# Kernel tuning notes

Measured on AMD Instinct MI355X. Metric: run time of the kernel, lower is better.

## Reference

```python
import jax, jax.numpy as jnp
import numpy as np

# ADMM hyperparameters for mode='only_tv'
GAMMA_TV = 10.0
ALPHA = 5.0
LAMBDA_TV = 1e-4
N_ITERS = 50


def soft_thresh(v, t):
    return jnp.sign(v) * jnp.maximum(jnp.abs(v) - t, 0.0)


def setup_inputs() -> dict:
    key = jax.random.key(0)
    k1, k2, k3 = jax.random.split(key, 3)
    target = jax.random.normal(k1, (4096,), dtype=jnp.float32)
    A = jax.random.normal(k2, (9, 4096), dtype=jnp.float32)  # [M, N], post-transpose
    x0 = jax.random.normal(k3, (4096,), dtype=jnp.float32)   # replaces torch.randn_like
    return {"target": target, "A": A, "x0": x0}


def reference(target, A, x0):
    N = A.shape[1]
    I = jnp.eye(N, dtype=A.dtype)
    Delta = jnp.roll(I, 1, axis=1) - I               # [N, N] circular difference
    DtD = Delta.T @ Delta
    AtA = A.T @ A
    # only_tv: gamma_l1 = beta = 0, so regularizer is ATA + gamma_tv*DtD + alpha*I
    inv_item = jnp.linalg.inv(AtA + GAMMA_TV * DtD + ALPHA * I)

    b = A @ target            # [M]
    bA = b @ A                # [N], constant across iterations

    def step(carry, _):
        x, eta_tv, tau = carry
        # u_tv: soft-threshold of backward difference (roll along axis 0)
        u_tv = soft_thresh(jnp.roll(x, 1, axis=0) - x + eta_tv / GAMMA_TV,
                           LAMBDA_TV / GAMMA_TV)
        # w: nonnegativity split variable
        w = jnp.maximum(x + tau / ALPHA, 0.0)
        # x-update (zero terms for l1/dwt/z dropped: gamma_l1 = gamma_dwt = beta = 0)
        resid = bA + (GAMMA_TV * u_tv - eta_tv) + (ALPHA * w - tau)
        x = resid @ inv_item
        # dual updates
        eta_tv = eta_tv + GAMMA_TV * (Delta @ x - u_tv)
        tau = tau + ALPHA * (x - w)
        return (x, eta_tv, tau), None

    zeros = jnp.zeros_like(x0)
    (x, _, _), _ = jax.lax.scan(step, (x0, zeros, zeros), None, length=N_ITERS)
    return x
```

## Files before the change

### kernel.cpp

```cpp
#include <hip/hip_runtime.h>
#include <math.h>

#define NT 512
#define EPT 8
#define NN 4096
#define MM 9
#define NIT 50
#define CJ 5

__device__ __forceinline__ void block_reduce9(const float pq[MM], float* __restrict__ s_part,
                                              float* __restrict__ dest, int destStride,
                                              int identCol, int t) {
#pragma unroll
  for (int m = 0; m < MM; ++m) s_part[m * NT + t] = pq[m];
  __syncthreads();
  const int wave = t >> 6, lane = t & 63;
  for (int m = wave; m < MM; m += NT / 64) {
    float s = 0.f;
#pragma unroll
    for (int k = 0; k < NT / 64; ++k) s += s_part[m * NT + lane + 64 * k];
#pragma unroll
    for (int off = 32; off; off >>= 1) s += __shfl_xor(s, off, 64);
    if (lane == 0) dest[m * destStride] = s + ((m == identCol) ? 1.f : 0.f);
  }
  __syncthreads();
}

__device__ __forceinline__ void solveM(const float r[EPT], float p[EPT],
                                       float* __restrict__ s_lastA,
                                       float* __restrict__ s_lastB, int t) {
  float yl[EPT];
  yl[EPT - 1] = r[EPT - 1] * 0.1f;
#pragma unroll
  for (int j = EPT - 2; j >= 0; --j) yl[j] = fmaf(0.5f, yl[j + 1], r[j] * 0.1f);
  s_lastA[t] = yl[0];
  __syncthreads();
  float c = 0.f, wgt = 1.f;
#pragma unroll
  for (int j = 0; j < CJ; ++j) { c = fmaf(wgt, s_lastA[(t + 1 + j) & (NT - 1)], c); wgt *= (1.f / 256.f); }
  float y[EPT];
  float f = 0.5f;
#pragma unroll
  for (int j = EPT - 1; j >= 0; --j) { y[j] = fmaf(c, f, yl[j]); f *= 0.5f; }
  float pl[EPT];
  pl[0] = 0.5f * y[0];
#pragma unroll
  for (int j = 1; j < EPT; ++j) pl[j] = 0.5f * (y[j] + pl[j - 1]);
  s_lastB[t] = pl[EPT - 1];
  __syncthreads();
  float c2 = 0.f, w2 = 1.f;
#pragma unroll
  for (int j = 0; j < CJ; ++j) { c2 = fmaf(w2, s_lastB[(t + NT - 1 - j) & (NT - 1)], c2); w2 *= (1.f / 256.f); }
  float f2 = 0.5f;
#pragma unroll
  for (int j = 0; j < EPT; ++j) { p[j] = fmaf(c2, f2, pl[j]); f2 *= 0.5f; }
}

__global__ void __launch_bounds__(NT)
admm_kernel(const float* __restrict__ tg, const float* __restrict__ Ag,
            const float* __restrict__ x0, float* __restrict__ out) {
  __shared__ float s_x[NN];
  __shared__ float s_part[MM * NT];
  __shared__ float s_lastA[NT];
  __shared__ float s_lastB[NT];
  __shared__ float s_q[MM];
  __shared__ float s_z[MM];
  __shared__ float s_S[MM * MM];
  __shared__ float s_Sinv[MM * MM];

  const int t = threadIdx.x;
  const int base = t * EPT;

  float A[MM][EPT];
#pragma unroll
  for (int m = 0; m < MM; ++m) {
    float4 a0 = *(const float4*)(Ag + m * NN + base);
    float4 a1 = *(const float4*)(Ag + m * NN + base + 4);
    A[m][0] = a0.x; A[m][1] = a0.y; A[m][2] = a0.z; A[m][3] = a0.w;
    A[m][4] = a1.x; A[m][5] = a1.y; A[m][6] = a1.z; A[m][7] = a1.w;
  }

  float x[EPT], tgt[EPT];
  {
    float4 v0 = *(const float4*)(x0 + base);
    float4 v1 = *(const float4*)(x0 + base + 4);
    x[0] = v0.x; x[1] = v0.y; x[2] = v0.z; x[3] = v0.w;
    x[4] = v1.x; x[5] = v1.y; x[6] = v1.z; x[7] = v1.w;
    float4 t0 = *(const float4*)(tg + base);
    float4 t1 = *(const float4*)(tg + base + 4);
    tgt[0] = t0.x; tgt[1] = t0.y; tgt[2] = t0.z; tgt[3] = t0.w;
    tgt[4] = t1.x; tgt[5] = t1.y; tgt[6] = t1.z; tgt[7] = t1.w;
  }
#pragma unroll
  for (int j = 0; j < EPT; ++j) s_x[base + j] = x[j];

  float pq[MM];
#pragma unroll
  for (int m = 0; m < MM; ++m) {
    float s = 0.f;
#pragma unroll
    for (int j = 0; j < EPT; ++j) s = fmaf(A[m][j], tgt[j], s);
    pq[m] = s;
  }
  block_reduce9(pq, s_part, s_q, 1, -1, t);

  float bA[EPT];
  {
    float bv[MM];
#pragma unroll
    for (int m = 0; m < MM; ++m) bv[m] = s_q[m];
#pragma unroll
    for (int j = 0; j < EPT; ++j) {
      float s = 0.f;
#pragma unroll
      for (int m = 0; m < MM; ++m) s = fmaf(bv[m], A[m][j], s);
      bA[j] = s;
    }
  }

  float G[MM][EPT];
#pragma unroll
  for (int m = 0; m < MM; ++m) {
    float rin[EPT], pcol[EPT];
#pragma unroll
    for (int j = 0; j < EPT; ++j) rin[j] = A[m][j];
    solveM(rin, pcol, s_lastA, s_lastB, t);
#pragma unroll
    for (int j = 0; j < EPT; ++j) G[m][j] = pcol[j];
  }

#pragma unroll
  for (int mcol = 0; mcol < MM; ++mcol) {
#pragma unroll
    for (int k = 0; k < MM; ++k) {
      float s = 0.f;
#pragma unroll
      for (int j = 0; j < EPT; ++j) s = fmaf(A[k][j], G[mcol][j], s);
      pq[k] = s;
    }
    block_reduce9(pq, s_part, &s_S[mcol], MM, mcol, t);
  }

  if (t < 64) {
    float row[2 * MM];
#pragma unroll
    for (int j = 0; j < MM; ++j) row[j] = (t < MM) ? s_S[t * MM + j] : 0.f;
#pragma unroll
    for (int j = 0; j < MM; ++j) row[MM + j] = (j == t) ? 1.f : 0.f;
#pragma unroll
    for (int pp = 0; pp < MM; ++pp) {
      float pr[2 * MM];
#pragma unroll
      for (int j = 0; j < 2 * MM; ++j) pr[j] = __shfl(row[j], pp, 64);
      float rpiv = 1.f / pr[pp];
      float fct = row[pp] * rpiv;
#pragma unroll
      for (int j = 0; j < 2 * MM; ++j)
        row[j] = (t == pp) ? pr[j] * rpiv : fmaf(-fct, pr[j], row[j]);
    }
    if (t < MM) {
#pragma unroll
      for (int j = 0; j < MM; ++j) s_Sinv[t * MM + j] = row[MM + j];
    }
  }
  __syncthreads();

  float eta[EPT], tau[EPT];
#pragma unroll
  for (int j = 0; j < EPT; ++j) { eta[j] = 0.f; tau[j] = 0.f; }

#pragma unroll 1
  for (int it = 0; it < NIT; ++it) {
    float xm1 = s_x[(base + NN - 1) & (NN - 1)];
    float u[EPT], w[EPT], r[EPT];
#pragma unroll
    for (int j = 0; j < EPT; ++j) {
      float xprev = (j == 0) ? xm1 : x[j - 1];
      float v = xprev - x[j] + eta[j] * 0.1f;
      float a = fabsf(v) - 1e-5f;
      u[j] = (a > 0.f) ? copysignf(a, v) : 0.f;
      w[j] = fmaxf(fmaf(tau[j], 0.2f, x[j]), 0.f);
      r[j] = bA[j] + 10.f * u[j] - eta[j] + 5.f * w[j] - tau[j];
    }
    float p[EPT];
    solveM(r, p, s_lastA, s_lastB, t);
#pragma unroll
    for (int m = 0; m < MM; ++m) {
      float s = 0.f;
#pragma unroll
      for (int j = 0; j < EPT; ++j) s = fmaf(A[m][j], p[j], s);
      pq[m] = s;
    }
    block_reduce9(pq, s_part, s_q, 1, -1, t);
    if (t < MM) {
      float s = 0.f;
#pragma unroll
      for (int k = 0; k < MM; ++k) s = fmaf(s_Sinv[t * MM + k], s_q[k], s);
      s_z[t] = s;
    }
    __syncthreads();
    float zz[MM];
#pragma unroll
    for (int m = 0; m < MM; ++m) zz[m] = s_z[m];
    float xn[EPT];
#pragma unroll
    for (int j = 0; j < EPT; ++j) {
      float s = p[j];
#pragma unroll
      for (int m = 0; m < MM; ++m) s = fmaf(-G[m][j], zz[m], s);
      xn[j] = s;
    }
#pragma unroll
    for (int j = 0; j < EPT; ++j) s_x[base + j] = xn[j];
    __syncthreads();
    float xnext = s_x[(base + EPT) & (NN - 1)];
#pragma unroll
    for (int j = 0; j < EPT; ++j) {
      float d = ((j == EPT - 1) ? xnext : xn[j + 1]) - xn[j];
      eta[j] = fmaf(10.f, d - u[j], eta[j]);
      tau[j] = fmaf(5.f, xn[j] - w[j], tau[j]);
      x[j] = xn[j];
    }
  }

  float4 o0, o1;
  o0.x = x[0]; o0.y = x[1]; o0.z = x[2]; o0.w = x[3];
  o1.x = x[4]; o1.y = x[5]; o1.z = x[6]; o1.w = x[7];
  *(float4*)(out + base) = o0;
  *(float4*)(out + base + 4) = o1;
}

extern "C" void kernel_launch(void* const* d_in, const int* in_sizes, int n_in,
                              void* d_out, int out_size, void* d_ws, size_t ws_size,
                              hipStream_t stream) {
  const float* target = (const float*)d_in[0];
  const float* A      = (const float*)d_in[1];
  const float* x0     = (const float*)d_in[2];
  admm_kernel<<<1, NT, 0, stream>>>(target, A, x0, (float*)d_out);
}
```

Baseline: 120.8 us.

## Fuse tridiagonal solve passes and fold Sinv into G to cut barriers

Rewrites the per-thread banded solve so both scan passes publish their partial carries with one shared-memory exchange and one barrier instead of two. Precomputes G·Sinv once before the loop, which removes the per-iteration 9x9 matvec and its extra barrier. The per-iteration 9-way reduction now uses wave shuffles followed by a single barrier, with every thread summing the eight wave partials. It also alternates scratch buffers during setup, changes launch bounds and stops unrolling the S-build loop, at the cost of more shuffle instructions and slightly different floating-point rounding.

```diff
diff --git a/kernel.cpp b/kernel.cpp
--- a/kernel.cpp
+++ b/kernel.cpp
@@ -6,7 +6,11 @@
 #define NN 4096
 #define MM 9
 #define NIT 50
-#define CJ 5
+
+#define W256_1 3.90625e-3f
+#define W256_2 1.52587890625e-5f
+#define W256_3 5.9604644775390625e-8f
+#define K1LAST 0.3333282470703125f
 
 __device__ __forceinline__ void block_reduce9(const float pq[MM], float* __restrict__ s_part,
                                               float* __restrict__ dest, int destStride,
@@ -26,50 +30,54 @@
   __syncthreads();
 }
 
-__device__ __forceinline__ void solveM(const float r[EPT], float p[EPT],
-                                       float* __restrict__ s_lastA,
-                                       float* __restrict__ s_lastB, int t) {
+__device__ __forceinline__ void solveM_fused(const float r[EPT], float p[EPT],
+                                             float2* __restrict__ s_sc, int t) {
+  const float K1[EPT] = {0.001953125f, 0.0048828125f, 0.01025390625f, 0.020751953125f,
+                         0.0416259765625f, 0.08331298828125f, 0.166656494140625f,
+                         0.3333282470703125f};
   float yl[EPT];
   yl[EPT - 1] = r[EPT - 1] * 0.1f;
 #pragma unroll
   for (int j = EPT - 2; j >= 0; --j) yl[j] = fmaf(0.5f, yl[j + 1], r[j] * 0.1f);
-  s_lastA[t] = yl[0];
-  __syncthreads();
-  float c = 0.f, wgt = 1.f;
-#pragma unroll
-  for (int j = 0; j < CJ; ++j) { c = fmaf(wgt, s_lastA[(t + 1 + j) & (NT - 1)], c); wgt *= (1.f / 256.f); }
-  float y[EPT];
-  float f = 0.5f;
-#pragma unroll
-  for (int j = EPT - 1; j >= 0; --j) { y[j] = fmaf(c, f, yl[j]); f *= 0.5f; }
-  float pl[EPT];
-  pl[0] = 0.5f * y[0];
-#pragma unroll
-  for (int j = 1; j < EPT; ++j) pl[j] = 0.5f * (y[j] + pl[j - 1]);
-  s_lastB[t] = pl[EPT - 1];
-  __syncthreads();
-  float c2 = 0.f, w2 = 1.f;
-#pragma unroll
-  for (int j = 0; j < CJ; ++j) { c2 = fmaf(w2, s_lastB[(t + NT - 1 - j) & (NT - 1)], c2); w2 *= (1.f / 256.f); }
+  float pl0[EPT];
+  pl0[0] = 0.5f * yl[0];
+#pragma unroll
+  for (int j = 1; j < EPT; ++j) pl0[j] = 0.5f * (yl[j] + pl0[j - 1]);
+  s_sc[t] = make_float2(yl[0], pl0[EPT - 1]);
+  __syncthreads();
+  float2 g[9];
+#pragma unroll
+  for (int k = 0; k < 9; ++k) g[k] = s_sc[(t + k - 4) & (NT - 1)];
+  float c = fmaf(W256_3, g[8].x, fmaf(W256_2, g[7].x, fmaf(W256_1, g[6].x, g[5].x)));
+  float s1 = fmaf(W256_3, g[0].y, fmaf(W256_2, g[1].y, fmaf(W256_1, g[2].y, g[3].y)));
+  float s2 = g[4].x;
+  s2 = fmaf(W256_1, g[3].x + g[5].x, s2);
+  s2 = fmaf(W256_2, g[2].x + g[6].x, s2);
+  s2 = fmaf(W256_3, g[1].x + g[7].x, s2);
+  float c2 = fmaf(K1LAST, s2, s1);
   float f2 = 0.5f;
 #pragma unroll
-  for (int j = 0; j < EPT; ++j) { p[j] = fmaf(c2, f2, pl[j]); f2 *= 0.5f; }
-}
-
-__global__ void __launch_bounds__(NT)
+  for (int j = 0; j < EPT; ++j) {
+    p[j] = fmaf(c2, f2, fmaf(c, K1[j], pl0[j]));
+    f2 *= 0.5f;
+  }
+}
+
+__global__ void __launch_bounds__(NT, 2)
 admm_kernel(const float* __restrict__ tg, const float* __restrict__ Ag,
             const float* __restrict__ x0, float* __restrict__ out) {
   __shared__ float s_x[NN];
   __shared__ float s_part[MM * NT];
-  __shared__ float s_lastA[NT];
-  __shared__ float s_lastB[NT];
+  __shared__ float2 s_sc[NT];
+  __shared__ float2 s_sc2[NT];
+  __shared__ float s_wq[8][12];
   __shared__ float s_q[MM];
-  __shared__ float s_z[MM];
   __shared__ float s_S[MM * MM];
   __shared__ float s_Sinv[MM * MM];
 
   const int t = threadIdx.x;
   const int base = t * EPT;
+  const int lane = t & 63, wave = t >> 6;
 
   float A[MM][EPT];
 #pragma unroll
@@ -124,12 +132,12 @@
     float rin[EPT], pcol[EPT];
 #pragma unroll
     for (int j = 0; j < EPT; ++j) rin[j] = A[m][j];
-    solveM(rin, pcol, s_lastA, s_lastB, t);
+    solveM_fused(rin, pcol, (m & 1) ? s_sc2 : s_sc, t);
 #pragma unroll
     for (int j = 0; j < EPT; ++j) G[m][j] = pcol[j];
   }
 
-#pragma unroll
+#pragma unroll 1
   for (int mcol = 0; mcol < MM; ++mcol) {
 #pragma unroll
     for (int k = 0; k < MM; ++k) {
@@ -164,6 +172,20 @@
     }
   }
   __syncthreads();
+
+#pragma unroll
+  for (int j = 0; j < EPT; ++j) {
+    float tmp[MM];
+#pragma unroll
+    for (int k = 0; k < MM; ++k) tmp[k] = G[k][j];
+#pragma unroll
+    for (int m = 0; m < MM; ++m) {
+      float s = 0.f;
+#pragma unroll
+      for (int k = 0; k < MM; ++k) s = fmaf(s_Sinv[k * MM + m], tmp[k], s);
+      G[m][j] = s;
+    }
+  }
 
   float eta[EPT], tau[EPT];
 #pragma unroll
@@ -183,7 +205,7 @@
       r[j] = bA[j] + 10.f * u[j] - eta[j] + 5.f * w[j] - tau[j];
     }
     float p[EPT];
-    solveM(r, p, s_lastA, s_lastB, t);
+    solveM_fused(r, p, s_sc, t);
 #pragma unroll
     for (int m = 0; m < MM; ++m) {
       float s = 0.f;
@@ -191,23 +213,38 @@
       for (int j = 0; j < EPT; ++j) s = fmaf(A[m][j], p[j], s);
       pq[m] = s;
     }
-    block_reduce9(pq, s_part, s_q, 1, -1, t);
-    if (t < MM) {
-      float s = 0.f;
-#pragma unroll
-      for (int k = 0; k < MM; ++k) s = fmaf(s_Sinv[t * MM + k], s_q[k], s);
-      s_z[t] = s;
+#pragma unroll
+    for (int off = 32; off; off >>= 1) {
+#pragma unroll
+      for (int m = 0; m < MM; ++m) pq[m] += __shfl_xor(pq[m], off, 64);
+    }
+    if (lane == 0) {
+#pragma unroll
+      for (int m = 0; m < MM; ++m) s_wq[wave][m] = pq[m];
     }
     __syncthreads();
-    float zz[MM];
-#pragma unroll
-    for (int m = 0; m < MM; ++m) zz[m] = s_z[m];
+    float q[MM];
+    {
+      float4 a0 = *(const float4*)&s_wq[0][0];
+      float4 a1 = *(const float4*)&s_wq[0][4];
+      float  a2 = s_wq[0][8];
+      q[0] = a0.x; q[1] = a0.y; q[2] = a0.z; q[3] = a0.w;
+      q[4] = a1.x; q[5] = a1.y; q[6] = a1.z; q[7] = a1.w; q[8] = a2;
+#pragma unroll
+      for (int wv = 1; wv < 8; ++wv) {
+        float4 b0 = *(const float4*)&s_wq[wv][0];
+        float4 b1 = *(const float4*)&s_wq[wv][4];
+        float  b2 = s_wq[wv][8];
+        q[0] += b0.x; q[1] += b0.y; q[2] += b0.z; q[3] += b0.w;
+        q[4] += b1.x; q[5] += b1.y; q[6] += b1.z; q[7] += b1.w; q[8] += b2;
+      }
+    }
     float xn[EPT];
 #pragma unroll
     for (int j = 0; j < EPT; ++j) {
       float s = p[j];
 #pragma unroll
-      for (int m = 0; m < MM; ++m) s = fmaf(-G[m][j], zz[m], s);
+      for (int m = 0; m < MM; ++m) s = fmaf(-G[m][j], q[m], s);
       xn[j] = s;
     }
 #pragma unroll
```

After: 165.9 us. 1.37x slower.
